# Performance work log

Hardware: AMD Instinct MI355X
Metric: run time of the kernel (lower is better)

## Reference

```python
import jax, jax.numpy as jnp
import numpy as np
import math

B, D, P = 32768, 4096, 16

def setup_inputs() -> dict:
    key = jax.random.key(0)
    ks = jax.random.split(key, 4)
    x = jax.random.normal(ks[0], (B, D), dtype=jnp.float32)
    # orthogonal-ish init: random normal rows scaled (exact orthogonality not needed for correctness baseline)
    W_refine = jax.random.normal(ks[1], (P, D), dtype=jnp.float32) / np.sqrt(D)
    W_out = jax.random.normal(ks[2], (P, D), dtype=jnp.float32) / np.sqrt(D)
    b_refine = jnp.zeros((P,), dtype=jnp.float32)
    b_out = jnp.zeros((P,), dtype=jnp.float32)
    gamma = jnp.ones((D,), dtype=jnp.float32)
    beta = jnp.zeros((D,), dtype=jnp.float32)
    return {"x": x, "W_refine": W_refine, "b_refine": b_refine,
            "W_out": W_out, "b_out": b_out, "gamma": gamma, "beta": beta}

def reference(x, W_refine, b_refine, W_out, b_out, gamma, beta):
    # phases in (-pi, pi)
    refine_phase = jnp.tanh(x @ W_refine.T + b_refine) * math.pi   # [B, P]
    output_phase = jnp.tanh(x @ W_out.T + b_out) * math.pi        # [B, P]
    # Since x is real: Re(e^{i r} * x * e^{-i o}) = x * cos(r - o)
    # phase_alignment = Re(e^{i(r-o)}) = cos(r - o)
    cosd = jnp.cos(refine_phase - output_phase)                    # [B, P]
    resonance = jnp.mean(cosd, axis=-1, keepdims=True)             # [B, 1]
    resonance_gain = jax.nn.softplus(resonance + 0.5)              # [B, 1]
    # summed = sum_p Re(bound_p * conj(output_phasor_p)) = x * sum_p cos(r_p - o_p)
    summed = x * jnp.sum(cosd, axis=-1, keepdims=True)             # [B, D]
    n_planes = W_refine.shape[0]
    output = summed * resonance_gain / n_planes                    # [B, D]
    # LayerNorm(output) with eps=1e-5 (torch default)
    mu = jnp.mean(output, axis=-1, keepdims=True)
    var = jnp.mean((output - mu) ** 2, axis=-1, keepdims=True)
    normed = (output - mu) * jax.lax.rsqrt(var + 1e-5) * gamma + beta
    return x + normed
```

## Files before the change

### kernel.cpp

```cpp
#include <hip/hip_runtime.h>
#include <math.h>


constexpr int Dh     = 4096;
constexpr int Ph     = 16;
constexpr int NPL    = 32;
constexpr int CHUNK  = 256;
constexpr int NCHUNK = Dh / CHUNK;
constexpr int RPB    = 8;
constexpr int NW     = 8;
constexpr int PPW    = NPL / NW;
constexpr int BLOCK  = 64 * NW;

__global__ __launch_bounds__(BLOCK, 2)
void phase_fused(const float* __restrict__ x,
                 const float* __restrict__ Wr,
                 const float* __restrict__ br,
                 const float* __restrict__ Wo,
                 const float* __restrict__ bo,
                 const float* __restrict__ gamma,
                 const float* __restrict__ beta,
                 float* __restrict__ out)
{
    __shared__ float dots_lds[RPB][NPL];
    __shared__ float stats_lds[RPB][2];
    __shared__ float scale_lds[RPB][2];

    const int t    = threadIdx.x;
    const int wv   = t >> 6;
    const int lane = t & 63;
    const size_t rowbase = (size_t)blockIdx.x * RPB;

    const float* xrow[RPB];
#pragma unroll
    for (int r = 0; r < RPB; ++r)
        xrow[r] = x + (rowbase + r) * (size_t)Dh + lane * 4;

    const float* wrow[PPW];
#pragma unroll
    for (int p = 0; p < PPW; ++p) {
        const int q = wv * PPW + p;
        wrow[p] = ((q < Ph) ? (Wr + (size_t)q * Dh) : (Wo + (size_t)(q - Ph) * Dh))
                  + lane * 4;
    }

    float acc[RPB][PPW];
#pragma unroll
    for (int r = 0; r < RPB; ++r)
#pragma unroll
        for (int p = 0; p < PPW; ++p) acc[r][p] = 0.f;
    float sx = 0.f, sxx = 0.f;

    for (int c = 0; c < NCHUNK; ++c) {
        const int off = c * CHUNK;
        float4 x4[RPB];
#pragma unroll
        for (int r = 0; r < RPB; ++r)
            x4[r] = *(const float4*)(xrow[r] + off);
        float4 w4[PPW];
#pragma unroll
        for (int p = 0; p < PPW; ++p)
            w4[p] = *(const float4*)(wrow[p] + off);

#pragma unroll
        for (int r = 0; r < RPB; ++r) {
            if (r == wv) {
                sx  += x4[r].x + x4[r].y + x4[r].z + x4[r].w;
                sxx += x4[r].x*x4[r].x + x4[r].y*x4[r].y
                     + x4[r].z*x4[r].z + x4[r].w*x4[r].w;
            }
#pragma unroll
            for (int p = 0; p < PPW; ++p)
                acc[r][p] += x4[r].x*w4[p].x + x4[r].y*w4[p].y
                           + x4[r].z*w4[p].z + x4[r].w*w4[p].w;
        }
    }

#pragma unroll
    for (int r = 0; r < RPB; ++r)
#pragma unroll
        for (int p = 0; p < PPW; ++p) {
            float v = acc[r][p];
#pragma unroll
            for (int m = 1; m < 64; m <<= 1) v += __shfl_xor(v, m, 64);
            if (lane == 0) dots_lds[r][wv * PPW + p] = v;
        }
#pragma unroll
    for (int m = 1; m < 64; m <<= 1) {
        sx  += __shfl_xor(sx, m, 64);
        sxx += __shfl_xor(sxx, m, 64);
    }
    if (lane == 0) { stats_lds[wv][0] = sx; stats_lds[wv][1] = sxx; }
    __syncthreads();

    if (t < RPB * Ph) {
        const int r = t >> 4, p = t & 15;
        float d1 = dots_lds[r][p]      + br[p];
        float d2 = dots_lds[r][Ph + p] + bo[p];
        float cd = cosf((tanhf(d1) - tanhf(d2)) * 3.14159265358979323846f);
#pragma unroll
        for (int m = 1; m < 16; m <<= 1) cd += __shfl_xor(cd, m, 16);
        if (p == 0) {
            float s    = cd;
            float gain = log1pf(expf(s * (1.f / Ph) + 0.5f));
            float cm   = s * gain * (1.f / Ph);
            float mu   = stats_lds[r][0] * (1.f / Dh);
            float var  = stats_lds[r][1] * (1.f / Dh) - mu * mu;
            var = fmaxf(var, 0.f);
            float rstd  = rsqrtf(cm * cm * var + 1e-5f);
            float alpha = cm * rstd;
            scale_lds[r][0] = alpha;
            scale_lds[r][1] = alpha * mu;
        }
    }
    __syncthreads();

    {
        const int col0 = wv * 512 + lane * 4;
        const float4 g4a = *(const float4*)(gamma + col0);
        const float4 g4b = *(const float4*)(gamma + col0 + 256);
        const float4 b4a = *(const float4*)(beta  + col0);
        const float4 b4b = *(const float4*)(beta  + col0 + 256);
#pragma unroll
        for (int r = 0; r < RPB; ++r) {
            const float alpha = scale_lds[r][0];
            const float am    = scale_lds[r][1];
            const float* xr  = x   + (rowbase + r) * (size_t)Dh;
            float*       orw = out + (rowbase + r) * (size_t)Dh;
            float4 xa = *(const float4*)(xr + col0);
            float4 xb = *(const float4*)(xr + col0 + 256);
            float4 oa, ob;
            oa.x = xa.x + g4a.x * (alpha * xa.x - am) + b4a.x;
            oa.y = xa.y + g4a.y * (alpha * xa.y - am) + b4a.y;
            oa.z = xa.z + g4a.z * (alpha * xa.z - am) + b4a.z;
            oa.w = xa.w + g4a.w * (alpha * xa.w - am) + b4a.w;
            ob.x = xb.x + g4b.x * (alpha * xb.x - am) + b4b.x;
            ob.y = xb.y + g4b.y * (alpha * xb.y - am) + b4b.y;
            ob.z = xb.z + g4b.z * (alpha * xb.z - am) + b4b.z;
            ob.w = xb.w + g4b.w * (alpha * xb.w - am) + b4b.w;
            *(float4*)(orw + col0)       = oa;
            *(float4*)(orw + col0 + 256) = ob;
        }
    }
}

extern "C" void kernel_launch(void* const* d_in, const int* in_sizes, int n_in,
                              void* d_out, int out_size, void* d_ws, size_t ws_size,
                              hipStream_t stream)
{
    const float* x     = (const float*)d_in[0];
    const float* Wr    = (const float*)d_in[1];
    const float* br    = (const float*)d_in[2];
    const float* Wo    = (const float*)d_in[3];
    const float* bo    = (const float*)d_in[4];
    const float* gamma = (const float*)d_in[5];
    const float* beta  = (const float*)d_in[6];
    float* out = (float*)d_out;

    const int B = in_sizes[0] / Dh;
    dim3 grid(B / RPB);
    phase_fused<<<grid, BLOCK, 0, stream>>>(x, Wr, br, Wo, bo, gamma, beta, out);
}
```

Baseline: 388.4 us.

## Stage x rows into LDS with async global_load_lds double buffering

Each wave now loads only its own x row via direct global-to-LDS copies into a double-buffered shared tile covering four chunks. All waves then read the eight rows from LDS instead of each wave reading every row from global memory. This removes the 8x redundant global/L2 reads of x and overlaps the next group's loads with compute. It adds 64KB of LDS per block and a block-wide barrier per group, which may limit occupancy.

```diff
diff --git a/kernel.cpp b/kernel.cpp
--- a/kernel.cpp
+++ b/kernel.cpp
@@ -6,11 +6,19 @@
 constexpr int Ph     = 16;
 constexpr int NPL    = 32;
 constexpr int CHUNK  = 256;
-constexpr int NCHUNK = Dh / CHUNK;
+constexpr int GCHUNK = 4;
+constexpr int GCOLS  = CHUNK * GCHUNK;
+constexpr int NGRP   = Dh / GCOLS;
 constexpr int RPB    = 8;
 constexpr int NW     = 8;
 constexpr int PPW    = NPL / NW;
 constexpr int BLOCK  = 64 * NW;
+
+__device__ __forceinline__ void stage_chunk(const float* src, float* ldsdst) {
+    __builtin_amdgcn_global_load_lds(
+        (const __attribute__((address_space(1))) void*)src,
+        (__attribute__((address_space(3))) void*)ldsdst, 16, 0, 0);
+}
 
 __global__ __launch_bounds__(BLOCK, 2)
 void phase_fused(const float* __restrict__ x,
@@ -22,6 +30,7 @@
                  const float* __restrict__ beta,
                  float* __restrict__ out)
 {
+    __shared__ float x_lds[2][GCHUNK][RPB][CHUNK];
     __shared__ float dots_lds[RPB][NPL];
     __shared__ float stats_lds[RPB][2];
     __shared__ float scale_lds[RPB][2];
@@ -31,11 +40,6 @@
     const int lane = t & 63;
     const size_t rowbase = (size_t)blockIdx.x * RPB;
 
-    const float* xrow[RPB];
-#pragma unroll
-    for (int r = 0; r < RPB; ++r)
-        xrow[r] = x + (rowbase + r) * (size_t)Dh + lane * 4;
-
     const float* wrow[PPW];
 #pragma unroll
     for (int p = 0; p < PPW; ++p) {
@@ -43,6 +47,7 @@
         wrow[p] = ((q < Ph) ? (Wr + (size_t)q * Dh) : (Wo + (size_t)(q - Ph) * Dh))
                   + lane * 4;
     }
+    const float* xsrc = x + (rowbase + wv) * (size_t)Dh + lane * 4;
 
     float acc[RPB][PPW];
 #pragma unroll
@@ -51,29 +56,45 @@
         for (int p = 0; p < PPW; ++p) acc[r][p] = 0.f;
     float sx = 0.f, sxx = 0.f;
 
-    for (int c = 0; c < NCHUNK; ++c) {
-        const int off = c * CHUNK;
-        float4 x4[RPB];
 #pragma unroll
-        for (int r = 0; r < RPB; ++r)
-            x4[r] = *(const float4*)(xrow[r] + off);
-        float4 w4[PPW];
+    for (int k = 0; k < GCHUNK; ++k)
+        stage_chunk(xsrc + (size_t)k * CHUNK, &x_lds[0][k][wv][0]);
+    __syncthreads();
+
+    for (int g = 0; g < NGRP; ++g) {
+        if (g + 1 < NGRP) {
 #pragma unroll
-        for (int p = 0; p < PPW; ++p)
-            w4[p] = *(const float4*)(wrow[p] + off);
+            for (int k = 0; k < GCHUNK; ++k)
+                stage_chunk(xsrc + (size_t)((g + 1) * GCHUNK + k) * CHUNK,
+                            &x_lds[(g + 1) & 1][k][wv][0]);
+        }
+        const float* xb = &x_lds[g & 1][0][0][0];
+#pragma unroll
+        for (int k = 0; k < GCHUNK; ++k) {
+            const int off = (g * GCHUNK + k) * CHUNK;
+            float4 w4[PPW];
+#pragma unroll
+            for (int p = 0; p < PPW; ++p)
+                w4[p] = *(const float4*)(wrow[p] + off);
+            float4 x4[RPB];
+#pragma unroll
+            for (int r = 0; r < RPB; ++r)
+                x4[r] = *(const float4*)(xb + (k * RPB + r) * CHUNK + lane * 4);
 
 #pragma unroll
-        for (int r = 0; r < RPB; ++r) {
-            if (r == wv) {
-                sx  += x4[r].x + x4[r].y + x4[r].z + x4[r].w;
-                sxx += x4[r].x*x4[r].x + x4[r].y*x4[r].y
-                     + x4[r].z*x4[r].z + x4[r].w*x4[r].w;
+            for (int r = 0; r < RPB; ++r) {
+                if (r == wv) {
+                    sx  += x4[r].x + x4[r].y + x4[r].z + x4[r].w;
+                    sxx += x4[r].x*x4[r].x + x4[r].y*x4[r].y
+                         + x4[r].z*x4[r].z + x4[r].w*x4[r].w;
+                }
+#pragma unroll
+                for (int p = 0; p < PPW; ++p)
+                    acc[r][p] += x4[r].x*w4[p].x + x4[r].y*w4[p].y
+                               + x4[r].z*w4[p].z + x4[r].w*w4[p].w;
             }
-#pragma unroll
-            for (int p = 0; p < PPW; ++p)
-                acc[r][p] += x4[r].x*w4[p].x + x4[r].y*w4[p].y
-                           + x4[r].z*w4[p].z + x4[r].w*w4[p].w;
         }
+        __syncthreads();
     }
 
 #pragma unroll
```

Result: slower. 857.8 us (+120.9%).

## Stage x rows into LDS with async double-buffered global_load_lds

Applied to the files above, without the earlier changes.

Each wave now loads only its own row of x straight into LDS with the async global-to-LDS builtin, using a two-chunk group and double buffering. All waves then read all 8 rows from LDS, instead of every wave fetching all 8 rows from global memory. This removes the 8x redundant vector-memory traffic for x. The launch bound is also raised to 4 blocks per CU to add occupancy. The cost is about 32KB of LDS per block, a barrier per group, and a hand-unrolled schedule that relies on the barrier waiting for the async loads.

```diff
diff --git a/kernel.cpp b/kernel.cpp
--- a/kernel.cpp
+++ b/kernel.cpp
@@ -6,13 +6,20 @@
 constexpr int Ph     = 16;
 constexpr int NPL    = 32;
 constexpr int CHUNK  = 256;
-constexpr int NCHUNK = Dh / CHUNK;
+constexpr int GCH    = 2;
+constexpr int NGRP   = Dh / (CHUNK * GCH);
 constexpr int RPB    = 8;
 constexpr int NW     = 8;
 constexpr int PPW    = NPL / NW;
 constexpr int BLOCK  = 64 * NW;
 
-__global__ __launch_bounds__(BLOCK, 2)
+__device__ __forceinline__ void stage_chunk(const float* src, float* ldsdst) {
+    __builtin_amdgcn_global_load_lds(
+        (const __attribute__((address_space(1))) void*)src,
+        (__attribute__((address_space(3))) void*)ldsdst, 16, 0, 0);
+}
+
+__global__ __launch_bounds__(BLOCK, 4)
 void phase_fused(const float* __restrict__ x,
                  const float* __restrict__ Wr,
                  const float* __restrict__ br,
@@ -22,6 +29,7 @@
                  const float* __restrict__ beta,
                  float* __restrict__ out)
 {
+    __shared__ float x_lds[2][GCH][RPB][CHUNK];
     __shared__ float dots_lds[RPB][NPL];
     __shared__ float stats_lds[RPB][2];
     __shared__ float scale_lds[RPB][2];
@@ -31,11 +39,6 @@
     const int lane = t & 63;
     const size_t rowbase = (size_t)blockIdx.x * RPB;
 
-    const float* xrow[RPB];
-#pragma unroll
-    for (int r = 0; r < RPB; ++r)
-        xrow[r] = x + (rowbase + r) * (size_t)Dh + lane * 4;
-
     const float* wrow[PPW];
 #pragma unroll
     for (int p = 0; p < PPW; ++p) {
@@ -43,6 +46,7 @@
         wrow[p] = ((q < Ph) ? (Wr + (size_t)q * Dh) : (Wo + (size_t)(q - Ph) * Dh))
                   + lane * 4;
     }
+    const float* xsrc = x + (rowbase + wv) * (size_t)Dh + lane * 4;
 
     float acc[RPB][PPW];
 #pragma unroll
@@ -51,30 +55,58 @@
         for (int p = 0; p < PPW; ++p) acc[r][p] = 0.f;
     float sx = 0.f, sxx = 0.f;
 
-    for (int c = 0; c < NCHUNK; ++c) {
-        const int off = c * CHUNK;
-        float4 x4[RPB];
+    auto stage_group = [&](int g, int buf) {
 #pragma unroll
-        for (int r = 0; r < RPB; ++r)
-            x4[r] = *(const float4*)(xrow[r] + off);
-        float4 w4[PPW];
+        for (int k = 0; k < GCH; ++k)
+            stage_chunk(xsrc + (size_t)(g * GCH + k) * CHUNK,
+                        &x_lds[buf][k][wv][0]);
+    };
+
+    auto compute_group = [&](int g, int buf) {
+#pragma unroll 1
+        for (int k = 0; k < GCH; ++k) {
+            const int off = (g * GCH + k) * CHUNK;
+            float4 w4[PPW];
 #pragma unroll
-        for (int p = 0; p < PPW; ++p)
-            w4[p] = *(const float4*)(wrow[p] + off);
+            for (int p = 0; p < PPW; ++p)
+                w4[p] = *(const float4*)(wrow[p] + off);
+            float4 x4[RPB];
+#pragma unroll
+            for (int r = 0; r < RPB; ++r)
+                x4[r] = *(const float4*)(&x_lds[buf][k][r][lane * 4]);
 
 #pragma unroll
-        for (int r = 0; r < RPB; ++r) {
-            if (r == wv) {
-                sx  += x4[r].x + x4[r].y + x4[r].z + x4[r].w;
-                sxx += x4[r].x*x4[r].x + x4[r].y*x4[r].y
-                     + x4[r].z*x4[r].z + x4[r].w*x4[r].w;
+            for (int r = 0; r < RPB; ++r) {
+                if (r == wv) {
+                    sx  += x4[r].x + x4[r].y + x4[r].z + x4[r].w;
+                    sxx += x4[r].x*x4[r].x + x4[r].y*x4[r].y
+                         + x4[r].z*x4[r].z + x4[r].w*x4[r].w;
+                }
+#pragma unroll
+                for (int p = 0; p < PPW; ++p)
+                    acc[r][p] += x4[r].x*w4[p].x + x4[r].y*w4[p].y
+                               + x4[r].z*w4[p].z + x4[r].w*w4[p].w;
             }
-#pragma unroll
-            for (int p = 0; p < PPW; ++p)
-                acc[r][p] += x4[r].x*w4[p].x + x4[r].y*w4[p].y
-                           + x4[r].z*w4[p].z + x4[r].w*w4[p].w;
         }
-    }
+    };
+
+    stage_group(0, 0);
+    __syncthreads();
+    stage_group(1, 1); compute_group(0, 0);
+    __syncthreads();
+    stage_group(2, 0); compute_group(1, 1);
+    __syncthreads();
+    stage_group(3, 1); compute_group(2, 0);
+    __syncthreads();
+    stage_group(4, 0); compute_group(3, 1);
+    __syncthreads();
+    stage_group(5, 1); compute_group(4, 0);
+    __syncthreads();
+    stage_group(6, 0); compute_group(5, 1);
+    __syncthreads();
+    stage_group(7, 1); compute_group(6, 0);
+    __syncthreads();
+    compute_group(7, 1);
 
 #pragma unroll
     for (int r = 0; r < RPB; ++r)
```

Result: faster. 353.9 us (-8.9%).
